# Kernel tuning notes

Hardware: AMD Instinct MI355X
Metric: run time of the kernel (lower is better)

## Reference

```python
import jax, jax.numpy as jnp
import numpy as np


def setup_inputs() -> dict:
    key = jax.random.key(0)
    k1, k2, k3, k4, k5, k6 = jax.random.split(key, 6)
    B, N, D, H = 32, 4096, 256, 256
    return {
        "queries": jax.random.normal(k1, (B, N, D), dtype=jnp.float32),
        "keys": jax.random.normal(k2, (B, N, D), dtype=jnp.float32),
        "values": jax.random.normal(k3, (B, N, D), dtype=jnp.float32),
        "Wq": jax.random.normal(k4, (H, D), dtype=jnp.float32) * (1.0 / np.sqrt(D)),
        "Wk": jax.random.normal(k5, (H, D), dtype=jnp.float32) * (1.0 / np.sqrt(D)),
        "Wv": jax.random.normal(k6, (1, H), dtype=jnp.float32) * (1.0 / np.sqrt(H)),
    }


def reference(queries, keys, values, Wq, Wk, Wv):
    # Project queries and keys to hidden dim (torch Linear weight is [out, in])
    q = jnp.einsum('bnd,hd->bnh', queries, Wq)   # [B, N, H]
    k = jnp.einsum('bnd,hd->bnh', keys, Wk)      # [B, N, H]
    features = jnp.tanh(q + k)                   # [B, N, H]
    scores = jnp.einsum('bnh,oh->bno', features, Wv)  # [B, N, 1]
    alpha = jax.nn.softmax(scores, axis=1)       # softmax over N
    # dropout p=0 -> identity
    aggr_max = jnp.argmax(alpha, axis=1)         # [B, 1]
    out = jnp.sum(alpha * values, axis=1)        # [B, D]
    return (out, aggr_max)
```

## Files before the change

### kernel.cpp

```cpp
#include <hip/hip_runtime.h>

#define Bb 32
#define Nn 4096
#define Dd 256
#define Hh 256
#define NCH 32
#define CHUNK 128
#define NSTEPS 16

typedef __attribute__((ext_vector_type(8))) _Float16 half8;
typedef __attribute__((ext_vector_type(4))) float f32x4;

__device__ __forceinline__ float fast_tanhf(float x) {
    float e = __expf(2.0f * x);
    return 1.0f - 2.0f / (e + 1.0f);
}

__device__ __forceinline__ half8 cvt8(f32x4 v0, f32x4 v1) {
    half8 h;
    h[0] = (_Float16)v0.x; h[1] = (_Float16)v0.y;
    h[2] = (_Float16)v0.z; h[3] = (_Float16)v0.w;
    h[4] = (_Float16)v1.x; h[5] = (_Float16)v1.y;
    h[6] = (_Float16)v1.z; h[7] = (_Float16)v1.w;
    return h;
}

__global__ __launch_bounds__(256) void prep_w_kernel(
    const float* __restrict__ Wq, const float* __restrict__ Wk,
    _Float16* __restrict__ Wf)
{
    const int g = blockIdx.x * 256 + threadIdx.x;
    const int s = g >> 10;
    const int j = (g >> 6) & 15;
    const int l = g & 63;
    const int n = j * 16 + (l & 15);
    const int k = s * 32 + (l >> 4) * 8;
    const float* src = (k < 256) ? (Wq + n * 256 + k) : (Wk + n * 256 + (k - 256));
    const f32x4 v0 = *(const f32x4*)src;
    const f32x4 v1 = *(const f32x4*)(src + 4);
    *(half8*)&Wf[(size_t)g * 8] = cvt8(v0, v1);
}

__global__ __launch_bounds__(256, 2) void scores_mfma_kernel(
    const float* __restrict__ Q, const float* __restrict__ Kmat,
    const _Float16* __restrict__ Wf,
    const float* __restrict__ Wv, float* __restrict__ scores)
{
    __shared__ _Float16 Ahf[3][4096];
    __shared__ float red[4][128];

    const int tid = threadIdx.x;
    const int lane = tid & 63;
    const int wave = tid >> 6;
    const size_t row0 = (size_t)blockIdx.x * 128;

    f32x4 acc[8][4];
#pragma unroll
    for (int m = 0; m < 8; ++m)
#pragma unroll
        for (int n = 0; n < 4; ++n) acc[m][n] = (f32x4){0.f, 0.f, 0.f, 0.f};

    float wv[4];
#pragma unroll
    for (int n = 0; n < 4; ++n) wv[n] = Wv[wave * 64 + n * 16 + (lane & 15)];

    const int r_s0 = ((tid >> 6) << 4) + (tid & 15);
    const int r_s1 = r_s0 + 64;
    const int k_s0 = ((tid >> 4) & 3) * 8;

    f32x4 pA0, pA1, pA2, pA3;
    f32x4 qA0, qA1, qA2, qA3;
    half8 BA[4], BB[4];

    auto issue_aP = [&](int s) {
        const float* Asrc = (s < 8) ? Q : Kmat;
        const int kb = (s & 7) * 32 + k_s0;
        const float* p0 = Asrc + (row0 + r_s0) * Dd + kb;
        const float* p1 = Asrc + (row0 + r_s1) * Dd + kb;
        pA0 = *(const f32x4*)p0; pA1 = *(const f32x4*)(p0 + 4);
        pA2 = *(const f32x4*)p1; pA3 = *(const f32x4*)(p1 + 4);
    };
    auto issue_aQ = [&](int s) {
        const float* Asrc = (s < 8) ? Q : Kmat;
        const int kb = (s & 7) * 32 + k_s0;
        const float* p0 = Asrc + (row0 + r_s0) * Dd + kb;
        const float* p1 = Asrc + (row0 + r_s1) * Dd + kb;
        qA0 = *(const f32x4*)p0; qA1 = *(const f32x4*)(p0 + 4);
        qA2 = *(const f32x4*)p1; qA3 = *(const f32x4*)(p1 + 4);
    };
    auto issue_bA = [&](int s) {
#pragma unroll
        for (int n = 0; n < 4; ++n)
            BA[n] = *(const half8*)(Wf + ((size_t)(s * 16 + wave * 4 + n) * 64 + lane) * 8);
    };
    auto issue_bB = [&](int s) {
#pragma unroll
        for (int n = 0; n < 4; ++n)
            BB[n] = *(const half8*)(Wf + ((size_t)(s * 16 + wave * 4 + n) * 64 + lane) * 8);
    };
    auto storeP = [&](int buf) {
        *(half8*)&Ahf[buf][tid * 8] = cvt8(pA0, pA1);
        *(half8*)&Ahf[buf][(tid + 256) * 8] = cvt8(pA2, pA3);
    };
    auto storeQ = [&](int buf) {
        *(half8*)&Ahf[buf][tid * 8] = cvt8(qA0, qA1);
        *(half8*)&Ahf[buf][(tid + 256) * 8] = cvt8(qA2, qA3);
    };
    auto clusterA = [&](int rb) {
        __builtin_amdgcn_s_setprio(1);
#pragma unroll
        for (int m = 0; m < 8; ++m) {
            const half8 ahm = *(const half8*)&Ahf[rb][(m * 64 + lane) * 8];
#pragma unroll
            for (int n = 0; n < 4; ++n)
                acc[m][n] = __builtin_amdgcn_mfma_f32_16x16x32_f16(ahm, BA[n], acc[m][n], 0, 0, 0);
        }
        __builtin_amdgcn_s_setprio(0);
    };
    auto clusterB = [&](int rb) {
        __builtin_amdgcn_s_setprio(1);
#pragma unroll
        for (int m = 0; m < 8; ++m) {
            const half8 ahm = *(const half8*)&Ahf[rb][(m * 64 + lane) * 8];
#pragma unroll
            for (int n = 0; n < 4; ++n)
                acc[m][n] = __builtin_amdgcn_mfma_f32_16x16x32_f16(ahm, BB[n], acc[m][n], 0, 0, 0);
        }
        __builtin_amdgcn_s_setprio(0);
    };

    issue_aP(0);
    issue_aQ(1);
    issue_bA(0);
    storeP(0);
    __syncthreads();

    int rb = 0;
    for (int s2 = 0; s2 < 7; ++s2) {
        const int s = 2 * s2;
        const int rb1 = (rb == 2) ? 0 : rb + 1;
        const int rb2 = (rb1 == 2) ? 0 : rb1 + 1;
        issue_bB(s + 1);
        issue_aP(s + 2);
        clusterA(rb);
        storeQ(rb1);
        __syncthreads();
        issue_bA(s + 2);
        issue_aQ(s + 3);
        clusterB(rb1);
        storeP(rb2);
        __syncthreads();
        rb = rb2;
    }
    issue_bB(15);
    clusterA(2);
    storeQ(0);
    __syncthreads();
    clusterB(0);

    const int q = lane >> 4;
    float rp[8][4];
#pragma unroll
    for (int m = 0; m < 8; ++m)
#pragma unroll
        for (int r = 0; r < 4; ++r) {
            float v = 0.f;
#pragma unroll
            for (int n = 0; n < 4; ++n)
                v += wv[n] * fast_tanhf(acc[m][n][r]);
            rp[m][r] = v;
        }
#pragma unroll
    for (int mask = 1; mask <= 8; mask <<= 1)
#pragma unroll
        for (int m = 0; m < 8; ++m)
#pragma unroll
            for (int r = 0; r < 4; ++r)
                rp[m][r] += __shfl_xor(rp[m][r], mask, 64);

    if ((lane & 15) == 0) {
#pragma unroll
        for (int m = 0; m < 8; ++m)
#pragma unroll
            for (int r = 0; r < 4; ++r)
                red[wave][m * 16 + q * 4 + r] = rp[m][r];
    }
    __syncthreads();
    if (tid < 128)
        scores[row0 + tid] = (red[0][tid] + red[1][tid]) + (red[2][tid] + red[3][tid]);
}

#define MAXC 64
__global__ __launch_bounds__(256) void softmax_reduce_kernel(
    const float* __restrict__ scores,
    const float* __restrict__ Qg, const float* __restrict__ Kg,
    const float* __restrict__ Wq, const float* __restrict__ Wk,
    const float* __restrict__ Wv,
    float* __restrict__ mbuf, float* __restrict__ zbuf, float* __restrict__ out)
{
    __shared__ float sv[256];
    __shared__ int si[256];
    __shared__ double dred[256];
    __shared__ int cand[MAXC];
    __shared__ int cnt;
    const int b = blockIdx.x;
    const int tid = threadIdx.x;
    const float* sc = scores + (size_t)b * Nn;

    float best = -1e30f; int bi = 0;
    for (int j = 0; j < Nn / 256; ++j) {
        const int n = tid + j * 256;
        const float v = sc[n];
        if (v > best) { best = v; bi = n; }
    }
    sv[tid] = best; si[tid] = bi;
    __syncthreads();
    for (int off = 128; off > 0; off >>= 1) {
        if (tid < off) {
            const float v2 = sv[tid + off]; const int i2 = si[tid + off];
            if (v2 > sv[tid] || (v2 == sv[tid] && i2 < si[tid])) { sv[tid] = v2; si[tid] = i2; }
        }
        __syncthreads();
    }
    const float m = sv[0];
    int amax = si[0];
    __syncthreads();

    float ssum = 0.f;
    for (int j = 0; j < Nn / 256; ++j) ssum += __expf(sc[tid + j * 256] - m);
    sv[tid] = ssum;
    __syncthreads();
    for (int off = 128; off > 0; off >>= 1) {
        if (tid < off) sv[tid] += sv[tid + off];
        __syncthreads();
    }
    const float Z = sv[0];
    __syncthreads();

    if (tid == 0) cnt = 0;
    __syncthreads();
    const float tau = 0.008f;
    for (int j = 0; j < Nn / 256; ++j) {
        const int n = tid + j * 256;
        if (sc[n] >= m - tau) {
            const int p = atomicAdd(&cnt, 1);
            if (p < MAXC) cand[p] = n;
        }
    }
    __syncthreads();
    const int ncand = (cnt < MAXC) ? cnt : MAXC;
    if (ncand > 1) {
        double bestv = -1e300; int besti = 0x7fffffff;
        for (int c = 0; c < ncand; ++c) {
            const int n = cand[c];
            const float* qr = Qg + ((size_t)b * Nn + n) * Dd;
            const float* kr = Kg + ((size_t)b * Nn + n) * Dd;
            const float* wqr = Wq + tid * Dd;
            const float* wkr = Wk + tid * Dd;
            double accd = 0.0;
            for (int k2 = 0; k2 < Dd; ++k2)
                accd += (double)qr[k2] * (double)wqr[k2] + (double)kr[k2] * (double)wkr[k2];
            dred[tid] = (double)Wv[tid] * tanh(accd);
            __syncthreads();
            for (int off = 128; off > 0; off >>= 1) {
                if (tid < off) dred[tid] += dred[tid + off];
                __syncthreads();
            }
            const double s_c = dred[0];
            __syncthreads();
            if (s_c > bestv || (s_c == bestv && n < besti)) { bestv = s_c; besti = n; }
        }
        amax = besti;
    }

    if (tid == 0) {
        mbuf[b] = m;
        zbuf[b] = Z;
        out[(size_t)Bb * Dd + b] = (float)amax;
    }
}

__global__ __launch_bounds__(256) void partial_kernel(
    const float* __restrict__ V, const float* __restrict__ scores,
    const float* __restrict__ mbuf, float* __restrict__ part)
{
    __shared__ float e[CHUNK];
    const int c = blockIdx.x;
    const int b = blockIdx.y;
    const int tid = threadIdx.x;
    const float m = mbuf[b];
    if (tid < CHUNK)
        e[tid] = __expf(scores[(size_t)b * Nn + (size_t)c * CHUNK + tid] - m);
    __syncthreads();

    const float* vp = V + ((size_t)b * Nn + (size_t)c * CHUNK) * Dd + tid;
    float a0 = 0.f, a1 = 0.f, a2 = 0.f, a3 = 0.f;
    for (int n = 0; n < CHUNK; n += 4) {
        a0 = fmaf(e[n + 0], vp[(size_t)(n + 0) * Dd], a0);
        a1 = fmaf(e[n + 1], vp[(size_t)(n + 1) * Dd], a1);
        a2 = fmaf(e[n + 2], vp[(size_t)(n + 2) * Dd], a2);
        a3 = fmaf(e[n + 3], vp[(size_t)(n + 3) * Dd], a3);
    }
    part[((size_t)b * NCH + c) * Dd + tid] = ((a0 + a1) + (a2 + a3));
}

__global__ __launch_bounds__(256) void finalize_kernel(
    const float* __restrict__ part, const float* __restrict__ zbuf,
    float* __restrict__ out)
{
    const int b = blockIdx.x;
    const int tid = threadIdx.x;
    float s = 0.f;
#pragma unroll
    for (int c = 0; c < NCH; ++c) s += part[((size_t)b * NCH + c) * Dd + tid];
    out[(size_t)b * Dd + tid] = s / zbuf[b];
}

extern "C" void kernel_launch(void* const* d_in, const int* in_sizes, int n_in,
                              void* d_out, int out_size, void* d_ws, size_t ws_size,
                              hipStream_t stream) {
    const float* Q  = (const float*)d_in[0];
    const float* K  = (const float*)d_in[1];
    const float* V  = (const float*)d_in[2];
    const float* Wq = (const float*)d_in[3];
    const float* Wk = (const float*)d_in[4];
    const float* Wv = (const float*)d_in[5];
    float* out = (float*)d_out;

    char* wsb = (char*)d_ws;
    _Float16* Wf  = (_Float16*)(wsb);
    float* scores = (float*)(wsb + 262144);
    float* mbuf   = (float*)(wsb + 786432);
    float* zbuf   = (float*)(wsb + 786432 + 128);
    float* part   = (float*)(wsb + 786432 + 256);

    prep_w_kernel<<<dim3(64), dim3(256), 0, stream>>>(Wq, Wk, Wf);
    scores_mfma_kernel<<<dim3((Bb * Nn) / 128), dim3(256), 0, stream>>>(Q, K, Wf, Wv, scores);
    softmax_reduce_kernel<<<dim3(Bb), dim3(256), 0, stream>>>(scores, Q, K, Wq, Wk, Wv, mbuf, zbuf, out);
    partial_kernel<<<dim3(NCH, Bb), dim3(256), 0, stream>>>(V, scores, mbuf, part);
    finalize_kernel<<<dim3(Bb), dim3(256), 0, stream>>>(part, zbuf, out);
}
```

Baseline: 123.3 us.

## Keep projection weights in registers and stream activations directly into MFMA

The scores kernel drops the LDS triple-buffered A tiles and moves to 512-thread blocks. Each wave keeps its 32-column slice of the fp16 weight matrix resident in registers. Activations are read straight from global memory, converted to fp16 and fed into MFMAs one 16-row group at a time, which removes LDS traffic and block barriers. The cost is heavy register pressure (32 half8 values per lane), and each lane now issues small strided global loads. The near-tie tolerance for the exact argmax recheck is also widened, which may produce more candidates to recompute.

```diff
diff --git a/kernel.cpp b/kernel.cpp
--- a/kernel.cpp
+++ b/kernel.cpp
@@ -6,7 +6,6 @@
 #define Hh 256
 #define NCH 32
 #define CHUNK 128
-#define NSTEPS 16
 
 typedef __attribute__((ext_vector_type(8))) _Float16 half8;
 typedef __attribute__((ext_vector_type(4))) float f32x4;
@@ -41,153 +40,66 @@
     *(half8*)&Wf[(size_t)g * 8] = cvt8(v0, v1);
 }
 
-__global__ __launch_bounds__(256, 2) void scores_mfma_kernel(
+__global__ __launch_bounds__(512, 2) void scores_stream_kernel(
     const float* __restrict__ Q, const float* __restrict__ Kmat,
     const _Float16* __restrict__ Wf,
     const float* __restrict__ Wv, float* __restrict__ scores)
 {
-    __shared__ _Float16 Ahf[3][4096];
-    __shared__ float red[4][128];
+    __shared__ float red[8][128];
 
     const int tid = threadIdx.x;
     const int lane = tid & 63;
     const int wave = tid >> 6;
     const size_t row0 = (size_t)blockIdx.x * 128;
 
-    f32x4 acc[8][4];
-#pragma unroll
-    for (int m = 0; m < 8; ++m)
-#pragma unroll
-        for (int n = 0; n < 4; ++n) acc[m][n] = (f32x4){0.f, 0.f, 0.f, 0.f};
-
-    float wv[4];
-#pragma unroll
-    for (int n = 0; n < 4; ++n) wv[n] = Wv[wave * 64 + n * 16 + (lane & 15)];
-
-    const int r_s0 = ((tid >> 6) << 4) + (tid & 15);
-    const int r_s1 = r_s0 + 64;
-    const int k_s0 = ((tid >> 4) & 3) * 8;
-
-    f32x4 pA0, pA1, pA2, pA3;
-    f32x4 qA0, qA1, qA2, qA3;
-    half8 BA[4], BB[4];
-
-    auto issue_aP = [&](int s) {
-        const float* Asrc = (s < 8) ? Q : Kmat;
-        const int kb = (s & 7) * 32 + k_s0;
-        const float* p0 = Asrc + (row0 + r_s0) * Dd + kb;
-        const float* p1 = Asrc + (row0 + r_s1) * Dd + kb;
-        pA0 = *(const f32x4*)p0; pA1 = *(const f32x4*)(p0 + 4);
-        pA2 = *(const f32x4*)p1; pA3 = *(const f32x4*)(p1 + 4);
-    };
-    auto issue_aQ = [&](int s) {
-        const float* Asrc = (s < 8) ? Q : Kmat;
-        const int kb = (s & 7) * 32 + k_s0;
-        const float* p0 = Asrc + (row0 + r_s0) * Dd + kb;
-        const float* p1 = Asrc + (row0 + r_s1) * Dd + kb;
-        qA0 = *(const f32x4*)p0; qA1 = *(const f32x4*)(p0 + 4);
-        qA2 = *(const f32x4*)p1; qA3 = *(const f32x4*)(p1 + 4);
-    };
-    auto issue_bA = [&](int s) {
-#pragma unroll
-        for (int n = 0; n < 4; ++n)
-            BA[n] = *(const half8*)(Wf + ((size_t)(s * 16 + wave * 4 + n) * 64 + lane) * 8);
-    };
-    auto issue_bB = [&](int s) {
-#pragma unroll
-        for (int n = 0; n < 4; ++n)
-            BB[n] = *(const half8*)(Wf + ((size_t)(s * 16 + wave * 4 + n) * 64 + lane) * 8);
-    };
-    auto storeP = [&](int buf) {
-        *(half8*)&Ahf[buf][tid * 8] = cvt8(pA0, pA1);
-        *(half8*)&Ahf[buf][(tid + 256) * 8] = cvt8(pA2, pA3);
-    };
-    auto storeQ = [&](int buf) {
-        *(half8*)&Ahf[buf][tid * 8] = cvt8(qA0, qA1);
-        *(half8*)&Ahf[buf][(tid + 256) * 8] = cvt8(qA2, qA3);
-    };
-    auto clusterA = [&](int rb) {
-        __builtin_amdgcn_s_setprio(1);
-#pragma unroll
-        for (int m = 0; m < 8; ++m) {
-            const half8 ahm = *(const half8*)&Ahf[rb][(m * 64 + lane) * 8];
-#pragma unroll
-            for (int n = 0; n < 4; ++n)
-                acc[m][n] = __builtin_amdgcn_mfma_f32_16x16x32_f16(ahm, BA[n], acc[m][n], 0, 0, 0);
-        }
-        __builtin_amdgcn_s_setprio(0);
-    };
-    auto clusterB = [&](int rb) {
-        __builtin_amdgcn_s_setprio(1);
-#pragma unroll
-        for (int m = 0; m < 8; ++m) {
-            const half8 ahm = *(const half8*)&Ahf[rb][(m * 64 + lane) * 8];
-#pragma unroll
-            for (int n = 0; n < 4; ++n)
-                acc[m][n] = __builtin_amdgcn_mfma_f32_16x16x32_f16(ahm, BB[n], acc[m][n], 0, 0, 0);
-        }
-        __builtin_amdgcn_s_setprio(0);
-    };
-
-    issue_aP(0);
-    issue_aQ(1);
-    issue_bA(0);
-    storeP(0);
-    __syncthreads();
-
-    int rb = 0;
-    for (int s2 = 0; s2 < 7; ++s2) {
-        const int s = 2 * s2;
-        const int rb1 = (rb == 2) ? 0 : rb + 1;
-        const int rb2 = (rb1 == 2) ? 0 : rb1 + 1;
-        issue_bB(s + 1);
-        issue_aP(s + 2);
-        clusterA(rb);
-        storeQ(rb1);
-        __syncthreads();
-        issue_bA(s + 2);
-        issue_aQ(s + 3);
-        clusterB(rb1);
-        storeP(rb2);
-        __syncthreads();
-        rb = rb2;
-    }
-    issue_bB(15);
-    clusterA(2);
-    storeQ(0);
-    __syncthreads();
-    clusterB(0);
-
-    const int q = lane >> 4;
-    float rp[8][4];
-#pragma unroll
-    for (int m = 0; m < 8; ++m)
-#pragma unroll
-        for (int r = 0; r < 4; ++r) {
-            float v = 0.f;
-#pragma unroll
-            for (int n = 0; n < 4; ++n)
-                v += wv[n] * fast_tanhf(acc[m][n][r]);
-            rp[m][r] = v;
-        }
-#pragma unroll
-    for (int mask = 1; mask <= 8; mask <<= 1)
-#pragma unroll
-        for (int m = 0; m < 8; ++m)
-#pragma unroll
-            for (int r = 0; r < 4; ++r)
-                rp[m][r] += __shfl_xor(rp[m][r], mask, 64);
-
-    if ((lane & 15) == 0) {
-#pragma unroll
-        for (int m = 0; m < 8; ++m)
-#pragma unroll
-            for (int r = 0; r < 4; ++r)
-                red[wave][m * 16 + q * 4 + r] = rp[m][r];
-    }
-    __syncthreads();
-    if (tid < 128)
-        scores[row0 + tid] = (red[0][tid] + red[1][tid]) + (red[2][tid] + red[3][tid]);
+    half8 Breg[32];
+#pragma unroll
+    for (int s = 0; s < 16; ++s) {
+        Breg[2 * s]     = *(const half8*)(Wf + ((size_t)(s * 16 + 2 * wave)     * 64 + lane) * 8);
+        Breg[2 * s + 1] = *(const half8*)(Wf + ((size_t)(s * 16 + 2 * wave + 1) * 64 + lane) * 8);
+    }
+    const float wv0 = Wv[wave * 32 + (lane & 15)];
+    const float wv1 = Wv[wave * 32 + 16 + (lane & 15)];
+
+    const int rlane = lane & 15;
+    const int koff  = (lane >> 4) * 8;
+
+    for (int rg = 0; rg < 8; ++rg) {
+        const float* qb = Q    + (row0 + rg * 16 + rlane) * Dd + koff;
+        const float* kb = Kmat + (row0 + rg * 16 + rlane) * Dd + koff;
+        f32x4 acc0 = (f32x4){0.f, 0.f, 0.f, 0.f};
+        f32x4 acc1 = (f32x4){0.f, 0.f, 0.f, 0.f};
+#pragma unroll
+        for (int s = 0; s < 16; ++s) {
+            const float* p = (s < 8) ? (qb + s * 32) : (kb + (s - 8) * 32);
+            const f32x4 v0 = *(const f32x4*)p;
+            const f32x4 v1 = *(const f32x4*)(p + 4);
+            const half8 a = cvt8(v0, v1);
+            acc0 = __builtin_amdgcn_mfma_f32_16x16x32_f16(a, Breg[2 * s],     acc0, 0, 0, 0);
+            acc1 = __builtin_amdgcn_mfma_f32_16x16x32_f16(a, Breg[2 * s + 1], acc1, 0, 0, 0);
+        }
+        float t[4];
+#pragma unroll
+        for (int i = 0; i < 4; ++i)
+            t[i] = wv0 * fast_tanhf(acc0[i]) + wv1 * fast_tanhf(acc1[i]);
+#pragma unroll
+        for (int mask = 1; mask <= 8; mask <<= 1)
+#pragma unroll
+            for (int i = 0; i < 4; ++i)
+                t[i] += __shfl_xor(t[i], mask, 64);
+        if ((lane & 15) == 0) {
+#pragma unroll
+            for (int i = 0; i < 4; ++i)
+                red[wave][rg * 16 + (lane >> 4) * 4 + i] = t[i];
+        }
+    }
+    __syncthreads();
+    if (tid < 128) {
+        float s = 0.f;
+#pragma unroll
+        for (int w = 0; w < 8; ++w) s += red[w][tid];
+        scores[row0 + tid] = s;
+    }
 }
 
 #define MAXC 64
@@ -239,7 +151,7 @@
 
     if (tid == 0) cnt = 0;
     __syncthreads();
-    const float tau = 0.008f;
+    const float tau = 0.02f;
     for (int j = 0; j < Nn / 256; ++j) {
         const int n = tid + j * 256;
         if (sc[n] >= m - tau) {
@@ -335,7 +247,7 @@
     float* part   = (float*)(wsb + 786432 + 256);
 
     prep_w_kernel<<<dim3(64), dim3(256), 0, stream>>>(Wq, Wk, Wf);
-    scores_mfma_kernel<<<dim3((Bb * Nn) / 128), dim3(256), 0, stream>>>(Q, K, Wf, Wv, scores);
+    scores_stream_kernel<<<dim3((Bb * Nn) / 128), dim3(512), 0, stream>>>(Q, K, Wf, Wv, scores);
     softmax_reduce_kernel<<<dim3(Bb), dim3(256), 0, stream>>>(scores, Q, K, Wq, Wk, Wv, mbuf, zbuf, out);
     partial_kernel<<<dim3(NCH, Bb), dim3(256), 0, stream>>>(V, scores, mbuf, part);
     finalize_kernel<<<dim3(Bb), dim3(256), 0, stream>>>(part, zbuf, out);
```

Measured after the change: 365.8 us. 197% more time.
